# Performance work log

Hardware: AMD Instinct MI355X
Metric: run time of the kernel (lower is better)

## Reference

```python
import jax, jax.numpy as jnp
import numpy as np

BN_EPS = 1e-5

def conv1x1(x, w, b):
    # x: [B,C,H,W], w: [O,C], b: [O]
    return jnp.einsum('bchw,oc->bohw', x, w) + b[None, :, None, None]

def bn_inf(x, gamma, beta, mean, var):
    inv = gamma / jnp.sqrt(var + BN_EPS)
    return (x - mean[None, :, None, None]) * inv[None, :, None, None] + beta[None, :, None, None]

def setup_inputs() -> dict:
    key = jax.random.key(0)
    ks = jax.random.split(key, 24)
    B, Fg, Fl, Fi = 8, 256, 256, 64
    H = W = 64
    c8 = Fi // 8
    d = {}
    d['g'] = jax.random.normal(ks[0], (B, Fg, H, W), jnp.float32)
    d['x'] = jax.random.normal(ks[1], (B, Fl, H, W), jnp.float32)
    # W_g: conv1x1 + BN
    d['Wg_w'] = jax.random.normal(ks[2], (Fi, Fg), jnp.float32) * (1.0 / np.sqrt(Fg))
    d['Wg_b'] = jax.random.normal(ks[3], (Fi,), jnp.float32) * 0.02
    d['bng_gamma'] = jax.random.uniform(ks[4], (Fi,), jnp.float32, 0.5, 1.5)
    d['bng_beta'] = jax.random.normal(ks[5], (Fi,), jnp.float32) * 0.1
    d['bng_mean'] = jax.random.normal(ks[6], (Fi,), jnp.float32) * 0.1
    d['bng_var'] = jax.random.uniform(ks[7], (Fi,), jnp.float32, 0.5, 1.5)
    # W_x: conv1x1 + BN
    d['Wx_w'] = jax.random.normal(ks[8], (Fi, Fl), jnp.float32) * (1.0 / np.sqrt(Fl))
    d['Wx_b'] = jax.random.normal(ks[9], (Fi,), jnp.float32) * 0.02
    d['bnx_gamma'] = jax.random.uniform(ks[10], (Fi,), jnp.float32, 0.5, 1.5)
    d['bnx_beta'] = jax.random.normal(ks[11], (Fi,), jnp.float32) * 0.1
    d['bnx_mean'] = jax.random.normal(ks[12], (Fi,), jnp.float32) * 0.1
    d['bnx_var'] = jax.random.uniform(ks[13], (Fi,), jnp.float32, 0.5, 1.5)
    # psi: conv1x1 (Fi->1) + BN(1) + sigmoid
    d['psi_w'] = jax.random.normal(ks[14], (1, Fi), jnp.float32) * (1.0 / np.sqrt(Fi))
    d['psi_b'] = jax.random.normal(ks[15], (1,), jnp.float32) * 0.02
    d['bnp_gamma'] = jax.random.uniform(ks[16], (1,), jnp.float32, 0.5, 1.5)
    d['bnp_beta'] = jax.random.normal(ks[17], (1,), jnp.float32) * 0.1
    d['bnp_mean'] = jax.random.normal(ks[18], (1,), jnp.float32) * 0.1
    d['bnp_var'] = jax.random.uniform(ks[19], (1,), jnp.float32, 0.5, 1.5)
    # PAM convs
    d['pb_w'] = jax.random.normal(ks[20], (c8, Fi), jnp.float32) * (1.0 / np.sqrt(Fi))
    d['pb_b'] = jnp.zeros((c8,), jnp.float32)
    d['pc_w'] = jax.random.normal(ks[21], (c8, Fi), jnp.float32) * (1.0 / np.sqrt(Fi))
    d['pc_b'] = jnp.zeros((c8,), jnp.float32)
    d['pd_w'] = jax.random.normal(ks[22], (Fi, Fi), jnp.float32) * (1.0 / np.sqrt(Fi))
    d['pd_b'] = jnp.zeros((Fi,), jnp.float32)
    # scalar gates (torch inits to 0; use small nonzero to exercise the path)
    d['alpha'] = jax.random.normal(ks[23], (1,), jnp.float32) * 0.05
    d['cam_beta'] = jax.random.normal(jax.random.fold_in(key, 99), (1,), jnp.float32) * 0.05
    return d

def _cam(psi, cam_beta):
    B, C, H, W = psi.shape
    feat = psi.reshape(B, C, H * W)                       # [B,C,HW]
    att = jnp.einsum('bcn,bdn->bcd', feat, feat)          # [B,C,C]
    att_new = jnp.max(att, axis=-1, keepdims=True) - att  # max-subtract trick
    att = jax.nn.softmax(att_new, axis=-1)
    out = jnp.einsum('bcd,bdn->bcn', att, feat).reshape(B, C, H, W)
    return cam_beta[0] * out + psi

def _pam(psi, pb_w, pb_b, pc_w, pc_b, pd_w, pd_b, alpha):
    B, C, H, W = psi.shape
    HW = H * W
    fb = conv1x1(psi, pb_w, pb_b).reshape(B, -1, HW)      # [B,C/8,HW]
    fc = conv1x1(psi, pc_w, pc_b).reshape(B, -1, HW)      # [B,C/8,HW]
    energy = jnp.einsum('bki,bkj->bij', fb, fc)           # [B,HW,HW]
    att = jax.nn.softmax(energy, axis=-1)
    fd = conv1x1(psi, pd_w, pd_b).reshape(B, C, HW)       # [B,C,HW]
    out = jnp.einsum('bcj,bij->bci', fd, att).reshape(B, C, H, W)
    return alpha[0] * out + psi

def reference(g, x, Wg_w, Wg_b, bng_gamma, bng_beta, bng_mean, bng_var,
              Wx_w, Wx_b, bnx_gamma, bnx_beta, bnx_mean, bnx_var,
              psi_w, psi_b, bnp_gamma, bnp_beta, bnp_mean, bnp_var,
              pb_w, pb_b, pc_w, pc_b, pd_w, pd_b, alpha, cam_beta):
    g1 = bn_inf(conv1x1(g, Wg_w, Wg_b), bng_gamma, bng_beta, bng_mean, bng_var)
    x1 = bn_inf(conv1x1(x, Wx_w, Wx_b), bnx_gamma, bnx_beta, bnx_mean, bnx_var)
    psi = jax.nn.relu(g1 + x1)                            # [B,F_int,H,W]
    cam = _cam(psi, cam_beta)
    pam = _pam(psi, pb_w, pb_b, pc_w, pc_b, pd_w, pd_b, alpha)
    gate = bn_inf(conv1x1(cam * pam, psi_w, psi_b), bnp_gamma, bnp_beta, bnp_mean, bnp_var)
    da = jax.nn.sigmoid(gate)                             # [B,1,H,W]
    return x * da
```

## Files before the change

### kernel.cpp

```cpp
#include <hip/hip_runtime.h>
#include <hip/hip_bf16.h>
#include <math.h>

#define BB 8
#define CIN 256
#define FI 64
#define HW 4096
#define C8 8
#define EPS 1e-5f
#define LOG2E 1.4426950408889634f

typedef __attribute__((ext_vector_type(8))) short bf16x8;
typedef __attribute__((ext_vector_type(4))) float f32x4;
typedef __attribute__((ext_vector_type(4))) unsigned u32x4;
typedef unsigned short u16;

static __device__ __forceinline__ u16 f2b(float x) {
    unsigned u = __builtin_bit_cast(unsigned, x);
    return (u16)((u + 0x8000u) >> 16);
}
static __device__ __forceinline__ unsigned pk2(float a, float b) {
    unsigned ua = __builtin_bit_cast(unsigned, a);
    unsigned ub = __builtin_bit_cast(unsigned, b);
    return ((ua + 0x8000u) >> 16) | ((ub + 0x8000u) & 0xffff0000u);
}
static __device__ __forceinline__ unsigned cvtpk(float a, float b) {
    unsigned r;
    asm("v_cvt_pk_bf16_f32 %0, %1, %2" : "=v"(r) : "v"(a), "v"(b));
    return r;
}
static __device__ __forceinline__ float b2f(u16 v) {
    return __builtin_bit_cast(float, ((unsigned)v) << 16);
}

__global__ __launch_bounds__(256) void k_prep(
    const float* __restrict__ Wg, const float* __restrict__ Wgb,
    const float* __restrict__ gg, const float* __restrict__ gbeta,
    const float* __restrict__ gm, const float* __restrict__ gv,
    const float* __restrict__ Wx, const float* __restrict__ Wxb,
    const float* __restrict__ xg, const float* __restrict__ xbeta,
    const float* __restrict__ xm, const float* __restrict__ xv,
    const float* __restrict__ pbw, const float* __restrict__ pbb,
    const float* __restrict__ pcw, const float* __restrict__ pcb,
    const float* __restrict__ pdw, const float* __restrict__ pdb,
    u16* __restrict__ Wp, float* __restrict__ Cp,
    u16* __restrict__ Wcat, float* __restrict__ bcat)
{
    const int gid = blockIdx.x * 256 + threadIdx.x;
    for (int idx = gid; idx < FI * 512; idx += 4096) {
        int o = idx >> 9, k = idx & 511;
        float s, w;
        if (k < 256) { s = gg[o] * rsqrtf(gv[o] + EPS); w = Wg[o * 256 + k]; }
        else         { s = xg[o] * rsqrtf(xv[o] + EPS); w = Wx[o * 256 + k - 256]; }
        Wp[idx] = f2b(w * s);
    }
    for (int idx = gid; idx < 80 * 64; idx += 4096) {
        int row = idx >> 6, col = idx & 63;
        float w;
        if (row < 8)       w = pbw[row * 64 + col] * LOG2E;
        else if (row < 16) w = pcw[(row - 8) * 64 + col];
        else               w = pdw[(row - 16) * 64 + col];
        Wcat[idx] = f2b(w);
    }
    if (blockIdx.x == 0) {
        int tid = threadIdx.x;
        if (tid < FI) {
            float ig = gg[tid] * rsqrtf(gv[tid] + EPS);
            float ix = xg[tid] * rsqrtf(xv[tid] + EPS);
            Cp[tid] = (Wgb[tid] - gm[tid]) * ig + gbeta[tid]
                    + (Wxb[tid] - xm[tid]) * ix + xbeta[tid];
        }
        if (tid >= 64 && tid < 144) {
            int r = tid - 64;
            float bv = (r < 8) ? pbb[r] * LOG2E : (r < 16 ? pcb[r - 8] : pdb[r - 16]);
            bcat[r] = bv;
        }
    }
}

__global__ __launch_bounds__(256) void k_psi(
    const float* __restrict__ g, const float* __restrict__ x,
    const u16* __restrict__ Wp, const float* __restrict__ Cp,
    const u16* __restrict__ Wcat, const float* __restrict__ bcat,
    u16* __restrict__ psiB, u16* __restrict__ psiLo,
    u16* __restrict__ fbcT, u16* __restrict__ fdB)
{
    const int tid  = threadIdx.x;
    const int lane = tid & 63;
    const int w    = tid >> 6;
    const int n    = lane & 15;
    const int quad = lane >> 4;
    const int b    = blockIdx.y;
    const int p0   = blockIdx.x * 64;

    __shared__ u16 InT[64][72];
    __shared__ u16 Tbc[64][16];

    f32x4 acc[4];
#pragma unroll
    for (int mt = 0; mt < 4; ++mt) acc[mt] = (f32x4){0.f, 0.f, 0.f, 0.f};

    const size_t pxoff = (size_t)p0 + w * 16 + n;
#pragma unroll
    for (int kc = 0; kc < 8; ++kc) {
        const float* src = (kc < 4) ? g : x;
        const int ch0 = (kc & 3) * 64;
        const float* base = src + ((size_t)b * CIN + ch0 + quad * 8) * HW + pxoff;
#pragma unroll
        for (int ks = 0; ks < 2; ++ks) {
            const float* bp = base + (size_t)(ks * 32) * HW;
            float f0 = bp[0 * HW], f1 = bp[1 * HW], f2 = bp[2 * HW], f3 = bp[3 * HW];
            float f4 = bp[4 * HW], f5 = bp[5 * HW], f6 = bp[6 * HW], f7 = bp[7 * HW];
            u32x4 t = {pk2(f0, f1), pk2(f2, f3), pk2(f4, f5), pk2(f6, f7)};
            bf16x8 bfrag = __builtin_bit_cast(bf16x8, t);
            const int kglob = kc * 64 + ks * 32;
#pragma unroll
            for (int mt = 0; mt < 4; ++mt) {
                bf16x8 af = *(const bf16x8*)&Wp[(mt * 16 + n) * 512 + kglob + quad * 8];
                acc[mt] = __builtin_amdgcn_mfma_f32_16x16x32_bf16(
                              af, bfrag, acc[mt], 0, 0, 0);
            }
        }
    }

    float pv[4][4];
#pragma unroll
    for (int mt = 0; mt < 4; ++mt)
#pragma unroll
        for (int r = 0; r < 4; ++r) {
            int c = mt * 16 + quad * 4 + r;
            float v = acc[mt][r] + Cp[c];
            v = v > 0.f ? v : 0.f;
            pv[mt][r] = v;
            u16 hb = f2b(v);
            size_t idx = ((size_t)b * FI + c) * HW + p0 + w * 16 + n;
            psiB[idx]  = hb;
            psiLo[idx] = f2b(v - b2f(hb));
        }
#pragma unroll
    for (int mt = 0; mt < 4; ++mt) {
        *(unsigned*)&InT[w * 16 + n][mt * 16 + quad * 4]     = cvtpk(pv[mt][0], pv[mt][1]);
        *(unsigned*)&InT[w * 16 + n][mt * 16 + quad * 4 + 2] = cvtpk(pv[mt][2], pv[mt][3]);
    }
    __syncthreads();

    f32x4 facc[5];
#pragma unroll
    for (int nt = 0; nt < 5; ++nt) facc[nt] = (f32x4){0.f, 0.f, 0.f, 0.f};
#pragma unroll
    for (int ks = 0; ks < 2; ++ks) {
        bf16x8 af = *(const bf16x8*)&InT[w * 16 + n][ks * 32 + quad * 8];
#pragma unroll
        for (int nt = 0; nt < 5; ++nt) {
            bf16x8 bf = *(const bf16x8*)&Wcat[(nt * 16 + n) * FI + ks * 32 + quad * 8];
            facc[nt] = __builtin_amdgcn_mfma_f32_16x16x32_bf16(af, bf, facc[nt], 0, 0, 0);
        }
    }
    __syncthreads();

    {
        float bias = bcat[n];
#pragma unroll
        for (int r = 0; r < 4; ++r)
            Tbc[w * 16 + quad * 4 + r][n] = f2b(facc[0][r] + bias);
    }
#pragma unroll
    for (int nt = 1; nt < 5; ++nt) {
        int ch = (nt - 1) * 16 + n;
        float bias = bcat[nt * 16 + n];
        *(unsigned*)&InT[ch][w * 16 + quad * 4]     = cvtpk(facc[nt][0] + bias, facc[nt][1] + bias);
        *(unsigned*)&InT[ch][w * 16 + quad * 4 + 2] = cvtpk(facc[nt][2] + bias, facc[nt][3] + bias);
    }
    __syncthreads();
    {
        int row = tid >> 2, part = tid & 3;
        uint2 v = *(const uint2*)&Tbc[row][part * 4];
        *(uint2*)&fbcT[((size_t)b * HW + p0 + row) * 16 + part * 4] = v;
    }
#pragma unroll
    for (int rep = 0; rep < 2; ++rep) {
        int t = rep * 256 + tid;
        int ch = t >> 3, seg = t & 7;
        bf16x8 v = *(const bf16x8*)&InT[ch][seg * 8];
        *(bf16x8*)&fdB[((size_t)b * FI + ch) * HW + p0 + seg * 8] = v;
    }
}

static __device__ __forceinline__ void gram_body(
    int tid, int s, int b, int zz,
    const u16* __restrict__ psiB, const u16* __restrict__ psiLo,
    float* __restrict__ Gp)
{
    const int lane = tid & 63;
    const int w    = tid >> 6;
    const int n    = lane & 15;
    const int quad = lane >> 4;

    f32x4 acc[2];
#pragma unroll
    for (int nt = 0; nt < 2; ++nt) acc[nt] = (f32x4){0.f, 0.f, 0.f, 0.f};

    for (int ks = 0; ks < 4; ++ks) {
        const int k0 = s * 128 + ks * 32;
        const size_t ra = ((size_t)b * FI + w * 16 + n) * HW + k0 + quad * 8;
        bf16x8 ah = *(const bf16x8*)&psiB[ra];
        bf16x8 al = *(const bf16x8*)&psiLo[ra];
#pragma unroll
        for (int nt = 0; nt < 2; ++nt) {
            const size_t rb = ((size_t)b * FI + zz * 32 + nt * 16 + n) * HW + k0 + quad * 8;
            bf16x8 bh = *(const bf16x8*)&psiB[rb];
            bf16x8 bl = *(const bf16x8*)&psiLo[rb];
            acc[nt] = __builtin_amdgcn_mfma_f32_16x16x32_bf16(ah, bh, acc[nt], 0, 0, 0);
            acc[nt] = __builtin_amdgcn_mfma_f32_16x16x32_bf16(ah, bl, acc[nt], 0, 0, 0);
            acc[nt] = __builtin_amdgcn_mfma_f32_16x16x32_bf16(al, bh, acc[nt], 0, 0, 0);
        }
    }
#pragma unroll
    for (int nt = 0; nt < 2; ++nt)
#pragma unroll
        for (int r = 0; r < 4; ++r) {
            int i = w * 16 + quad * 4 + r;
            Gp[(((size_t)s * 8 + b) * 64 + i) * 64 + zz * 32 + nt * 16 + n] = acc[nt][r];
        }
}

struct PamShared {
    u16 Ks[2][68][8];
    u16 Vs[2][64][64];
    u16 Ps[4][16][64];
};

template<int P>
static __device__ __forceinline__ void pam_body(
    PamShared& sh, int tid, int b, int i0, int p,
    const u16* __restrict__ fbcT, const u16* __restrict__ fdB,
    u16* __restrict__ Opart, float* __restrict__ ml)
{
    const int lane = tid & 63;
    const int w    = tid >> 6;
    const int n    = lane & 15;
    const int quad = lane >> 4;
    constexpr int JPER = 64 / P;
    const int jstart = p * JPER, jend = jstart + JPER;

    if (tid < 16) {
        ((unsigned*)&sh.Ks[0][64][0])[tid] = 0u;
        ((unsigned*)&sh.Ks[1][64][0])[tid] = 0u;
    }

    bf16x8 qfrag = {};
    if (quad == 0)
        qfrag = *(const bf16x8*)&fbcT[((size_t)b * HW + i0 + w * 16 + n) * 16];

    const int kkey = tid >> 1, khalf = tid & 1;
    const int vch  = tid >> 3, vseg  = tid & 7;
    const int vslot = (vseg ^ (vch & 7)) << 3;
    const int pswz  = n & 7;

    const u16* kp = fbcT + ((size_t)b * HW + jstart * 64) * 16 + 8;
    const u16* vp = fdB + (size_t)b * FI * HW + jstart * 64;

    uint2 kr0 = make_uint2(0u, 0u), kr1 = make_uint2(0u, 0u);
    bf16x8 v0a, v0b, v1a, v1b;
    if (tid < 128) {
        kr0 = *(const uint2*)(kp + (size_t)kkey * 16 + khalf * 4);
        kr1 = *(const uint2*)(kp + 1024 + (size_t)kkey * 16 + khalf * 4);
    }
    v0a = *(const bf16x8*)(vp + (size_t)vch * HW + vseg * 8);
    v0b = *(const bf16x8*)(vp + (size_t)(32 + vch) * HW + vseg * 8);
    v1a = *(const bf16x8*)(vp + 64 + (size_t)vch * HW + vseg * 8);
    v1b = *(const bf16x8*)(vp + 64 + (size_t)(32 + vch) * HW + vseg * 8);

    f32x4 oacc[4];
#pragma unroll
    for (int mt = 0; mt < 4; ++mt) oacc[mt] = (f32x4){0.f, 0.f, 0.f, 0.f};
    float m = -1e30f, l = 0.f;

#define PAM_STEP(BUF)                                                           \
    {                                                                           \
        f32x4 s[4];                                                             \
        __builtin_amdgcn_s_setprio(1);                                          \
        _Pragma("unroll")                                                       \
        for (int mt = 0; mt < 4; ++mt) {                                        \
            bf16x8 af = *(const bf16x8*)&sh.Ks[BUF][mt * 16 + n + quad][0];     \
            s[mt] = __builtin_amdgcn_mfma_f32_16x16x32_bf16(                    \
                        af, qfrag, (f32x4){0.f, 0.f, 0.f, 0.f}, 0, 0, 0);       \
        }                                                                       \
        __builtin_amdgcn_s_setprio(0);                                          \
        float cm = fmaxf(fmaxf(s[0][0], s[0][1]), s[0][2]);                     \
        cm = fmaxf(fmaxf(cm, s[0][3]), s[1][0]);                                \
        cm = fmaxf(fmaxf(cm, s[1][1]), s[1][2]);                                \
        cm = fmaxf(fmaxf(cm, s[1][3]), s[2][0]);                                \
        cm = fmaxf(fmaxf(cm, s[2][1]), s[2][2]);                                \
        cm = fmaxf(fmaxf(cm, s[2][3]), s[3][0]);                                \
        cm = fmaxf(fmaxf(cm, s[3][1]), s[3][2]);                                \
        cm = fmaxf(cm, s[3][3]);                                                \
        cm = fmaxf(cm, __shfl_xor(cm, 16));                                     \
        cm = fmaxf(cm, __shfl_xor(cm, 32));                                     \
        if (__any(cm > m + 8.f)) {                                              \
            float mnew  = fmaxf(m, cm);                                         \
            float scale = __builtin_amdgcn_exp2f(m - mnew);                     \
            l *= scale;                                                         \
            _Pragma("unroll")                                                   \
            for (int mt = 0; mt < 4; ++mt) {                                    \
                oacc[mt][0] *= scale; oacc[mt][1] *= scale;                     \
                oacc[mt][2] *= scale; oacc[mt][3] *= scale;                     \
            }                                                                   \
            m = mnew;                                                           \
        }                                                                       \
        float psum = 0.f;                                                       \
        unsigned pw[4][2];                                                      \
        _Pragma("unroll")                                                       \
        for (int mt = 0; mt < 4; ++mt) {                                        \
            float e0 = __builtin_amdgcn_exp2f(s[mt][0] - m);                    \
            float e1 = __builtin_amdgcn_exp2f(s[mt][1] - m);                    \
            float e2 = __builtin_amdgcn_exp2f(s[mt][2] - m);                    \
            float e3 = __builtin_amdgcn_exp2f(s[mt][3] - m);                    \
            psum += (e0 + e1) + (e2 + e3);                                      \
            pw[mt][0] = cvtpk(e0, e1);                                          \
            pw[mt][1] = cvtpk(e2, e3);                                          \
        }                                                                       \
        l += psum;                                                              \
        _Pragma("unroll")                                                       \
        for (int mt = 0; mt < 4; ++mt) {                                        \
            int so = (((mt * 2 + (quad >> 1)) ^ pswz) << 3) + ((quad & 1) << 2);\
            *(uint2*)&sh.Ps[w][n][so] = make_uint2(pw[mt][0], pw[mt][1]);       \
        }                                                                       \
        __builtin_amdgcn_s_setprio(1);                                          \
        _Pragma("unroll")                                                       \
        for (int k0 = 0; k0 < 2; ++k0) {                                        \
            bf16x8 pf = *(const bf16x8*)&sh.Ps[w][n][((k0 * 4 + quad) ^ pswz) << 3];\
            _Pragma("unroll")                                                   \
            for (int mt = 0; mt < 4; ++mt) {                                    \
                bf16x8 vf = *(const bf16x8*)                                    \
                    &sh.Vs[BUF][mt * 16 + n][((k0 * 4 + quad) ^ pswz) << 3];    \
                oacc[mt] = __builtin_amdgcn_mfma_f32_16x16x32_bf16(             \
                               vf, pf, oacc[mt], 0, 0, 0);                      \
            }                                                                   \
        }                                                                       \
        __builtin_amdgcn_s_setprio(0);                                          \
    }

    for (int jc = jstart; jc < jend; jc += 2) {
        if (tid < 128) *(uint2*)&sh.Ks[0][kkey][khalf * 4] = kr0;
        *(bf16x8*)&sh.Vs[0][vch][vslot]      = v0a;
        *(bf16x8*)&sh.Vs[0][32 + vch][vslot] = v0b;
        if (jc + 2 < jend) {
            if (tid < 128)
                kr0 = *(const uint2*)(kp + 2048 + (size_t)kkey * 16 + khalf * 4);
            v0a = *(const bf16x8*)(vp + 128 + (size_t)vch * HW + vseg * 8);
            v0b = *(const bf16x8*)(vp + 128 + (size_t)(32 + vch) * HW + vseg * 8);
        }
        __syncthreads();
        PAM_STEP(0)

        if (tid < 128) *(uint2*)&sh.Ks[1][kkey][khalf * 4] = kr1;
        *(bf16x8*)&sh.Vs[1][vch][vslot]      = v1a;
        *(bf16x8*)&sh.Vs[1][32 + vch][vslot] = v1b;
        if (jc + 3 < jend) {
            if (tid < 128)
                kr1 = *(const uint2*)(kp + 3072 + (size_t)kkey * 16 + khalf * 4);
            v1a = *(const bf16x8*)(vp + 192 + (size_t)vch * HW + vseg * 8);
            v1b = *(const bf16x8*)(vp + 192 + (size_t)(32 + vch) * HW + vseg * 8);
        }
        kp += 2048;
        vp += 128;
        __syncthreads();
        PAM_STEP(1)
    }
#undef PAM_STEP

    l += __shfl_xor(l, 16);
    l += __shfl_xor(l, 32);
    const float rl = 1.f / l;
#pragma unroll
    for (int mt = 0; mt < 4; ++mt)
#pragma unroll
        for (int r = 0; r < 4; ++r) {
            int c = mt * 16 + quad * 4 + r;
            Opart[(((size_t)p * 8 + b) * FI + c) * HW + i0 + w * 16 + n] =
                f2b(oacc[mt][r] * rl);
        }
    if (quad == 0)
        ((float2*)ml)[((size_t)p * 8 + b) * HW + i0 + w * 16 + n] = make_float2(m, l);
}

__global__ __launch_bounds__(256) void k_pamgram(
    const u16* __restrict__ fbcT, const u16* __restrict__ fdB,
    const u16* __restrict__ psiB, const u16* __restrict__ psiLo,
    u16* __restrict__ Opart, float* __restrict__ ml, float* __restrict__ Gp)
{
    __shared__ PamShared sh;
    const int bid = blockIdx.x;
    const int tid = threadIdx.x;
    if (bid < 512) {
        gram_body(tid, bid & 31, (bid >> 5) & 7, bid >> 8, psiB, psiLo, Gp);
    } else {
        const int pid = bid - 512;
        pam_body<2>(sh, tid, pid & 7, ((pid >> 3) & 63) * 64, pid >> 9,
                    fbcT, fdB, Opart, ml);
    }
}

__global__ __launch_bounds__(256) void k_gram(
    const u16* __restrict__ psiB, const u16* __restrict__ psiLo,
    float* __restrict__ Gp)
{
    gram_body(threadIdx.x, blockIdx.x, blockIdx.y, blockIdx.z, psiB, psiLo, Gp);
}
__global__ __launch_bounds__(256) void k_pam(
    const u16* __restrict__ fbcT, const u16* __restrict__ fdB,
    u16* __restrict__ Opart, float* __restrict__ ml)
{
    __shared__ PamShared sh;
    pam_body<2>(sh, threadIdx.x, blockIdx.x, blockIdx.y * 64, blockIdx.z,
                fbcT, fdB, Opart, ml);
}

__global__ __launch_bounds__(256) void k_camsm(
    const float* __restrict__ Gp, float* __restrict__ att)
{
    const int tid = threadIdx.x, tx = tid & 63, ty = tid >> 6;
    const int b = blockIdx.x, i = blockIdx.y;
    __shared__ float part[4][64];

    float gs = 0.f;
#pragma unroll
    for (int j = 0; j < 8; ++j) {
        int s = ty * 8 + j;
        gs += Gp[(((size_t)s * 8 + b) * 64 + i) * 64 + tx];
    }
    part[ty][tx] = gs;
    __syncthreads();
    if (tid < 64) {
        float gsum = part[0][tx] + part[1][tx] + part[2][tx] + part[3][tx];
        float M = gsum;
#pragma unroll
        for (int msk = 1; msk < 64; msk <<= 1) M = fmaxf(M, __shfl_xor(M, msk));
        float a = M - gsum;
        float m2 = a;
#pragma unroll
        for (int msk = 1; msk < 64; msk <<= 1) m2 = fmaxf(m2, __shfl_xor(m2, msk));
        float p = __expf(a - m2);
        float ssum = p;
#pragma unroll
        for (int msk = 1; msk < 64; msk <<= 1) ssum += __shfl_xor(ssum, msk);
        att[((size_t)b * 64 + i) * 64 + tx] = p / ssum;
    }
}

__global__ __launch_bounds__(256) void k_final(
    const u16* __restrict__ psiB, const u16* __restrict__ psiLo,
    const float* __restrict__ att,
    const u16* __restrict__ Opart, const float* __restrict__ ml,
    const float* __restrict__ x,
    const float* __restrict__ psiw, const float* __restrict__ psib,
    const float* __restrict__ pg, const float* __restrict__ pbeta,
    const float* __restrict__ pm, const float* __restrict__ pv,
    const float* __restrict__ alpha, const float* __restrict__ camb,
    float* __restrict__ out)
{
    const int tid  = threadIdx.x;
    const int lane = tid & 63;
    const int w    = tid >> 6;
    const int n    = lane & 15;
    const int quad = lane >> 4;
    const int b = blockIdx.y, p0 = blockIdx.x * 64;

    __shared__ u16 Abf[64][64];
    __shared__ u16 tpB[64][64];
    __shared__ u16 tpLo[64][64];
    __shared__ float Wc0[64], Wc1[64], Pw[64];
    __shared__ alignas(16) float daL[64];
    __shared__ float Zp[4][64];

    {
        int c = tid >> 2, seg = tid & 3;
        const float* ap = &att[((size_t)b * 64 + c) * 64 + seg * 16];
        float4 v0 = *(const float4*)(ap);
        float4 v1 = *(const float4*)(ap + 4);
        float4 v2 = *(const float4*)(ap + 8);
        float4 v3 = *(const float4*)(ap + 12);
        float vv[16] = {v0.x, v0.y, v0.z, v0.w, v1.x, v1.y, v1.z, v1.w,
                        v2.x, v2.y, v2.z, v2.w, v3.x, v3.y, v3.z, v3.w};
#pragma unroll
        for (int j = 0; j < 8; ++j) {
            int d0 = seg * 16 + j * 2;
            int phys = (((d0 >> 3) ^ (c & 7)) << 3) | (d0 & 7);
            *(unsigned*)&Abf[c][phys] = cvtpk(vv[2 * j], vv[2 * j + 1]);
        }
    }
    {
        int px = tid & 63, grp = tid >> 6;
#pragma unroll
        for (int cc = 0; cc < 16; cc += 2) {
            int c = grp * 16 + cc;
            size_t i0 = ((size_t)b * FI + c) * HW + p0 + px;
            unsigned hb = ((unsigned)psiB[i0]) | (((unsigned)psiB[i0 + HW]) << 16);
            unsigned lb = ((unsigned)psiLo[i0]) | (((unsigned)psiLo[i0 + HW]) << 16);
            int phys = (((c >> 3) ^ (px & 7)) << 3) | (c & 7);
            *(unsigned*)&tpB[px][phys]  = hb;
            *(unsigned*)&tpLo[px][phys] = lb;
        }
    }
    if (tid < 64) {
        Pw[tid] = psiw[tid];
        float2 ml0 = ((const float2*)ml)[((size_t)0 * 8 + b) * HW + p0 + tid];
        float2 ml1 = ((const float2*)ml)[((size_t)1 * 8 + b) * HW + p0 + tid];
        float M  = fmaxf(ml0.x, ml1.x);
        float w0 = ml0.y * __builtin_amdgcn_exp2f(ml0.x - M);
        float w1 = ml1.y * __builtin_amdgcn_exp2f(ml1.x - M);
        float winv = 1.f / (w0 + w1);
        Wc0[tid] = w0 * winv; Wc1[tid] = w1 * winv;
    }
    __syncthreads();

    f32x4 acc[4];
#pragma unroll
    for (int nt = 0; nt < 4; ++nt) acc[nt] = (f32x4){0.f, 0.f, 0.f, 0.f};
#pragma unroll
    for (int ks = 0; ks < 2; ++ks) {
        int arow = w * 16 + n;
        bf16x8 af = *(const bf16x8*)&Abf[arow][((ks * 4 + quad) ^ (arow & 7)) << 3];
#pragma unroll
        for (int nt = 0; nt < 4; ++nt) {
            int brow = nt * 16 + n;
            int boff = ((ks * 4 + quad) ^ (brow & 7)) << 3;
            bf16x8 bh = *(const bf16x8*)&tpB[brow][boff];
            bf16x8 bl = *(const bf16x8*)&tpLo[brow][boff];
            acc[nt] = __builtin_amdgcn_mfma_f32_16x16x32_bf16(af, bh, acc[nt], 0, 0, 0);
            acc[nt] = __builtin_amdgcn_mfma_f32_16x16x32_bf16(af, bl, acc[nt], 0, 0, 0);
        }
    }

    const float al = alpha[0], cb = camb[0];
    float z[4] = {0.f, 0.f, 0.f, 0.f};
#pragma unroll
    for (int nt = 0; nt < 4; ++nt) {
        int px = nt * 16 + n;
        float w0 = Wc0[px], w1 = Wc1[px];
#pragma unroll
        for (int r = 0; r < 4; ++r) {
            int c = w * 16 + quad * 4 + r;
            int phys = (((c >> 3) ^ (px & 7)) << 3) | (c & 7);
            float ps  = b2f(tpB[px][phys]) + b2f(tpLo[px][phys]);
            float cam = cb * acc[nt][r] + ps;
            float oa = w0 * b2f(Opart[(((size_t)0 * 8 + b) * FI + c) * HW + p0 + px])
                     + w1 * b2f(Opart[(((size_t)1 * 8 + b) * FI + c) * HW + p0 + px]);
            float pam = al * oa + ps;
            z[nt] += Pw[c] * (cam * pam);
        }
    }
#pragma unroll
    for (int nt = 0; nt < 4; ++nt) {
        z[nt] += __shfl_xor(z[nt], 16);
        z[nt] += __shfl_xor(z[nt], 32);
    }
    if (quad == 0) {
#pragma unroll
        for (int nt = 0; nt < 4; ++nt) Zp[w][nt * 16 + n] = z[nt];
    }
    __syncthreads();
    if (tid < 64) {
        float zt = Zp[0][tid] + Zp[1][tid] + Zp[2][tid] + Zp[3][tid] + psib[0];
        float inv = pg[0] * rsqrtf(pv[0] + EPS);
        float gate = (zt - pm[0]) * inv + pbeta[0];
        daL[tid] = 1.f / (1.f + __expf(-gate));
    }
    __syncthreads();

    {
        const int pxg = tid & 15, chb = tid >> 4;
        float4 daf = *(const float4*)&daL[pxg * 4];
#pragma unroll
        for (int r = 0; r < 16; ++r) {
            int cl = chb + 16 * r;
            size_t idx = ((size_t)b * CIN + cl) * HW + p0 + pxg * 4;
            float4 xv = *(const float4*)&x[idx];
            *(float4*)&out[idx] = make_float4(xv.x * daf.x, xv.y * daf.y,
                                              xv.z * daf.z, xv.w * daf.w);
        }
    }
}

extern "C" void kernel_launch(void* const* d_in, const int* in_sizes, int n_in,
                              void* d_out, int out_size, void* d_ws, size_t ws_size,
                              hipStream_t stream)
{
    const float* g     = (const float*)d_in[0];
    const float* x     = (const float*)d_in[1];
    const float* Wg_w  = (const float*)d_in[2];
    const float* Wg_b  = (const float*)d_in[3];
    const float* bng_g = (const float*)d_in[4];
    const float* bng_b = (const float*)d_in[5];
    const float* bng_m = (const float*)d_in[6];
    const float* bng_v = (const float*)d_in[7];
    const float* Wx_w  = (const float*)d_in[8];
    const float* Wx_b  = (const float*)d_in[9];
    const float* bnx_g = (const float*)d_in[10];
    const float* bnx_b = (const float*)d_in[11];
    const float* bnx_m = (const float*)d_in[12];
    const float* bnx_v = (const float*)d_in[13];
    const float* psi_w = (const float*)d_in[14];
    const float* psi_b = (const float*)d_in[15];
    const float* bnp_g = (const float*)d_in[16];
    const float* bnp_b = (const float*)d_in[17];
    const float* bnp_m = (const float*)d_in[18];
    const float* bnp_v = (const float*)d_in[19];
    const float* pb_w  = (const float*)d_in[20];
    const float* pb_b  = (const float*)d_in[21];
    const float* pc_w  = (const float*)d_in[22];
    const float* pc_b  = (const float*)d_in[23];
    const float* pd_w  = (const float*)d_in[24];
    const float* pd_b  = (const float*)d_in[25];
    const float* alpha = (const float*)d_in[26];
    const float* camb  = (const float*)d_in[27];
    float* out = (float*)d_out;

    float* ws   = (float*)d_ws;
    u16*  psiB  = (u16*)(ws);
    u16*  psiLo = (u16*)(ws + 1048576);
    u16*  fbcT  = (u16*)(ws + 2097152);
    u16*  fdB   = (u16*)(ws + 2359296);
    float* att  = ws + 3407872;
    u16*  Wp    = (u16*)(ws + 3440640);
    float* Cp   = ws + 3457024;
    u16*  Wcat  = (u16*)(ws + 3457088);
    float* bcat = ws + 3459648;
    float* mlws = ws + 3459744;
    float* Gp   = ws + 3590816;

    const bool fused = ws_size >= (size_t)6736544 * 4;
    u16* Opart = fused ? (u16*)(ws + 4639392)
                       : (u16*)(ws + 3590816);

    k_prep<<<dim3(16), 256, 0, stream>>>(Wg_w, Wg_b, bng_g, bng_b, bng_m, bng_v,
                                         Wx_w, Wx_b, bnx_g, bnx_b, bnx_m, bnx_v,
                                         pb_w, pb_b, pc_w, pc_b, pd_w, pd_b,
                                         Wp, Cp, Wcat, bcat);
    k_psi<<<dim3(64, 8), 256, 0, stream>>>(g, x, Wp, Cp, Wcat, bcat,
                                           psiB, psiLo, fbcT, fdB);
    if (fused) {
        k_pamgram<<<dim3(1536), 256, 0, stream>>>(fbcT, fdB, psiB, psiLo,
                                                  Opart, mlws, Gp);
        k_camsm<<<dim3(8, 64), 256, 0, stream>>>(Gp, att);
    } else {
        k_gram<<<dim3(32, 8, 2), 256, 0, stream>>>(psiB, psiLo, Gp);
        k_camsm<<<dim3(8, 64), 256, 0, stream>>>(Gp, att);
        k_pam<<<dim3(8, 64, 2), 256, 0, stream>>>(fbcT, fdB, Opart, mlws);
    }
    k_final<<<dim3(64, 8), 256, 0, stream>>>(psiB, psiLo, att, Opart, mlws, x,
                                             psi_w, psi_b, bnp_g, bnp_b, bnp_m, bnp_v,
                                             alpha, camb, out);
}
```

Measured before the change: 245.6 us.

## Emit pixel-major psi copy and add vectorized 32-pixel final kernel

k_psi now also writes a transposed, pixel-major copy of psi (hi and lo bf16 parts) through shared memory, so the final kernel can load psi with coalesced 16-byte reads. A new k_final_v processes 32 pixels per block, doubling the grid, uses XOR-swizzled shared tiles, and writes the output with float4 stores. The goal is cheaper, better-coalesced loads in the final stage, paid for by extra global writes in k_psi and a larger workspace. It falls back to the old path when the workspace is too small.

```diff
diff --git a/kernel.cpp b/kernel.cpp
--- a/kernel.cpp
+++ b/kernel.cpp
@@ -83,7 +83,8 @@
     const u16* __restrict__ Wp, const float* __restrict__ Cp,
     const u16* __restrict__ Wcat, const float* __restrict__ bcat,
     u16* __restrict__ psiB, u16* __restrict__ psiLo,
-    u16* __restrict__ fbcT, u16* __restrict__ fdB)
+    u16* __restrict__ fbcT, u16* __restrict__ fdB,
+    u16* __restrict__ psiT, u16* __restrict__ psiTLo)
 {
     const int tid  = threadIdx.x;
     const int lane = tid & 63;
@@ -94,6 +95,8 @@
     const int p0   = blockIdx.x * 64;
 
     __shared__ u16 InT[64][72];
+    __shared__ u16 TpH[64][72];
+    __shared__ u16 TpL[64][72];
     __shared__ u16 Tbc[64][16];
 
     f32x4 acc[4];
@@ -124,6 +127,7 @@
     }
 
     float pv[4][4];
+    unsigned hbv[4][4], lov[4][4];
 #pragma unroll
     for (int mt = 0; mt < 4; ++mt)
 #pragma unroll
@@ -133,16 +137,34 @@
             v = v > 0.f ? v : 0.f;
             pv[mt][r] = v;
             u16 hb = f2b(v);
+            u16 lo = f2b(v - b2f(hb));
+            hbv[mt][r] = hb;
+            lov[mt][r] = lo;
             size_t idx = ((size_t)b * FI + c) * HW + p0 + w * 16 + n;
             psiB[idx]  = hb;
-            psiLo[idx] = f2b(v - b2f(hb));
+            psiLo[idx] = lo;
         }
 #pragma unroll
     for (int mt = 0; mt < 4; ++mt) {
         *(unsigned*)&InT[w * 16 + n][mt * 16 + quad * 4]     = cvtpk(pv[mt][0], pv[mt][1]);
         *(unsigned*)&InT[w * 16 + n][mt * 16 + quad * 4 + 2] = cvtpk(pv[mt][2], pv[mt][3]);
-    }
-    __syncthreads();
+        *(unsigned*)&TpH[w * 16 + n][mt * 16 + quad * 4]     = hbv[mt][0] | (hbv[mt][1] << 16);
+        *(unsigned*)&TpH[w * 16 + n][mt * 16 + quad * 4 + 2] = hbv[mt][2] | (hbv[mt][3] << 16);
+        *(unsigned*)&TpL[w * 16 + n][mt * 16 + quad * 4]     = lov[mt][0] | (lov[mt][1] << 16);
+        *(unsigned*)&TpL[w * 16 + n][mt * 16 + quad * 4 + 2] = lov[mt][2] | (lov[mt][3] << 16);
+    }
+    __syncthreads();
+
+    if (psiT != nullptr) {
+#pragma unroll
+        for (int rep = 0; rep < 2; ++rep) {
+            int t = rep * 256 + tid;
+            int row = t >> 3, seg = t & 7;
+            size_t o = ((size_t)b * HW + p0 + row) * 64 + seg * 8;
+            *(bf16x8*)&psiT[o]   = *(const bf16x8*)&TpH[row][seg * 8];
+            *(bf16x8*)&psiTLo[o] = *(const bf16x8*)&TpL[row][seg * 8];
+        }
+    }
 
     f32x4 facc[5];
 #pragma unroll
@@ -449,7 +471,143 @@
     }
 }
 
-__global__ __launch_bounds__(256) void k_final(
+__global__ __launch_bounds__(256) void k_final_v(
+    const u16* __restrict__ psiT, const u16* __restrict__ psiTLo,
+    const float* __restrict__ att,
+    const u16* __restrict__ Opart, const float* __restrict__ ml,
+    const float* __restrict__ x,
+    const float* __restrict__ psiw, const float* __restrict__ psib,
+    const float* __restrict__ pg, const float* __restrict__ pbeta,
+    const float* __restrict__ pm, const float* __restrict__ pv,
+    const float* __restrict__ alpha, const float* __restrict__ camb,
+    float* __restrict__ out)
+{
+    const int tid  = threadIdx.x;
+    const int lane = tid & 63;
+    const int w    = tid >> 6;
+    const int n    = lane & 15;
+    const int quad = lane >> 4;
+    const int b = blockIdx.y, p0 = blockIdx.x * 32;
+
+    __shared__ u16 Abf[64][64];
+    __shared__ u16 tpB[32][64];
+    __shared__ u16 tpLo[32][64];
+    __shared__ u16 OpS[2][64][40];
+    __shared__ float Wc[2][32];
+    __shared__ float Pw[64];
+    __shared__ alignas(16) float daL[32];
+    __shared__ float Zp[4][32];
+
+    {
+        int c = tid >> 2, seg = tid & 3;
+        const float* ap = &att[((size_t)b * 64 + c) * 64 + seg * 16];
+        float4 v0 = *(const float4*)(ap);
+        float4 v1 = *(const float4*)(ap + 4);
+        float4 v2 = *(const float4*)(ap + 8);
+        float4 v3 = *(const float4*)(ap + 12);
+        float vv[16] = {v0.x, v0.y, v0.z, v0.w, v1.x, v1.y, v1.z, v1.w,
+                        v2.x, v2.y, v2.z, v2.w, v3.x, v3.y, v3.z, v3.w};
+#pragma unroll
+        for (int j = 0; j < 8; ++j) {
+            int d0 = seg * 16 + j * 2;
+            int phys = (((d0 >> 3) ^ (c & 7)) << 3) | (d0 & 7);
+            *(unsigned*)&Abf[c][phys] = cvtpk(vv[2 * j], vv[2 * j + 1]);
+        }
+    }
+    {
+        int row = tid >> 3, seg = tid & 7;
+        size_t o = ((size_t)b * HW + p0 + row) * 64 + seg * 8;
+        int phys = ((seg ^ (row & 7)) << 3);
+        *(bf16x8*)&tpB[row][phys]  = *(const bf16x8*)&psiT[o];
+        *(bf16x8*)&tpLo[row][phys] = *(const bf16x8*)&psiTLo[o];
+    }
+#pragma unroll
+    for (int rep = 0; rep < 2; ++rep) {
+        int cid = rep * 256 + tid;
+        int pp = cid >> 8, c = (cid >> 2) & 63, sg = cid & 3;
+        *(bf16x8*)&OpS[pp][c][sg * 8] =
+            *(const bf16x8*)&Opart[(((size_t)pp * 8 + b) * FI + c) * HW + p0 + sg * 8];
+    }
+    if (tid < 64) Pw[tid] = psiw[tid];
+    if (tid < 32) {
+        float2 ml0 = ((const float2*)ml)[((size_t)0 * 8 + b) * HW + p0 + tid];
+        float2 ml1 = ((const float2*)ml)[((size_t)1 * 8 + b) * HW + p0 + tid];
+        float M  = fmaxf(ml0.x, ml1.x);
+        float w0 = ml0.y * __builtin_amdgcn_exp2f(ml0.x - M);
+        float w1 = ml1.y * __builtin_amdgcn_exp2f(ml1.x - M);
+        float winv = 1.f / (w0 + w1);
+        Wc[0][tid] = w0 * winv; Wc[1][tid] = w1 * winv;
+    }
+    __syncthreads();
+
+    f32x4 acc[2];
+#pragma unroll
+    for (int nt = 0; nt < 2; ++nt) acc[nt] = (f32x4){0.f, 0.f, 0.f, 0.f};
+#pragma unroll
+    for (int ks = 0; ks < 2; ++ks) {
+        int arow = w * 16 + n;
+        bf16x8 af = *(const bf16x8*)&Abf[arow][((ks * 4 + quad) ^ (arow & 7)) << 3];
+#pragma unroll
+        for (int nt = 0; nt < 2; ++nt) {
+            int brow = nt * 16 + n;
+            int boff = ((ks * 4 + quad) ^ (brow & 7)) << 3;
+            bf16x8 bh = *(const bf16x8*)&tpB[brow][boff];
+            bf16x8 bl = *(const bf16x8*)&tpLo[brow][boff];
+            acc[nt] = __builtin_amdgcn_mfma_f32_16x16x32_bf16(af, bh, acc[nt], 0, 0, 0);
+            acc[nt] = __builtin_amdgcn_mfma_f32_16x16x32_bf16(af, bl, acc[nt], 0, 0, 0);
+        }
+    }
+
+    const float al = alpha[0], cb = camb[0];
+    float z[2] = {0.f, 0.f};
+#pragma unroll
+    for (int nt = 0; nt < 2; ++nt) {
+        int px = nt * 16 + n;
+        float w0 = Wc[0][px], w1 = Wc[1][px];
+#pragma unroll
+        for (int r = 0; r < 4; ++r) {
+            int c = w * 16 + quad * 4 + r;
+            int phys = (((c >> 3) ^ (px & 7)) << 3) | (c & 7);
+            float ps  = b2f(tpB[px][phys]) + b2f(tpLo[px][phys]);
+            float cam = cb * acc[nt][r] + ps;
+            float oa = w0 * b2f(OpS[0][c][px]) + w1 * b2f(OpS[1][c][px]);
+            float pam = al * oa + ps;
+            z[nt] += Pw[c] * (cam * pam);
+        }
+    }
+#pragma unroll
+    for (int nt = 0; nt < 2; ++nt) {
+        z[nt] += __shfl_xor(z[nt], 16);
+        z[nt] += __shfl_xor(z[nt], 32);
+    }
+    if (quad == 0) {
+#pragma unroll
+        for (int nt = 0; nt < 2; ++nt) Zp[w][nt * 16 + n] = z[nt];
+    }
+    __syncthreads();
+    if (tid < 32) {
+        float zt = Zp[0][tid] + Zp[1][tid] + Zp[2][tid] + Zp[3][tid] + psib[0];
+        float inv = pg[0] * rsqrtf(pv[0] + EPS);
+        float gate = (zt - pm[0]) * inv + pbeta[0];
+        daL[tid] = 1.f / (1.f + __expf(-gate));
+    }
+    __syncthreads();
+
+    {
+        const int pxg = tid & 7, chb = tid >> 3;
+        float4 daf = *(const float4*)&daL[pxg * 4];
+#pragma unroll
+        for (int r = 0; r < 8; ++r) {
+            int cl = chb + 32 * r;
+            size_t idx = ((size_t)b * CIN + cl) * HW + p0 + pxg * 4;
+            float4 xv = *(const float4*)&x[idx];
+            *(float4*)&out[idx] = make_float4(xv.x * daf.x, xv.y * daf.y,
+                                              xv.z * daf.z, xv.w * daf.w);
+        }
+    }
+}
+
+__global__ __launch_bounds__(256) void k_final_s(
     const u16* __restrict__ psiB, const u16* __restrict__ psiLo,
     const float* __restrict__ att,
     const u16* __restrict__ Opart, const float* __restrict__ ml,
@@ -618,29 +776,34 @@
     float* out = (float*)d_out;
 
     float* ws   = (float*)d_ws;
-    u16*  psiB  = (u16*)(ws);
-    u16*  psiLo = (u16*)(ws + 1048576);
-    u16*  fbcT  = (u16*)(ws + 2097152);
-    u16*  fdB   = (u16*)(ws + 2359296);
-    float* att  = ws + 3407872;
-    u16*  Wp    = (u16*)(ws + 3440640);
-    float* Cp   = ws + 3457024;
-    u16*  Wcat  = (u16*)(ws + 3457088);
-    float* bcat = ws + 3459648;
-    float* mlws = ws + 3459744;
-    float* Gp   = ws + 3590816;
-
-    const bool fused = ws_size >= (size_t)6736544 * 4;
-    u16* Opart = fused ? (u16*)(ws + 4639392)
-                       : (u16*)(ws + 3590816);
+    u16*  psiB   = (u16*)(ws);
+    u16*  psiLo  = (u16*)(ws + 1048576);
+    u16*  fbcT   = (u16*)(ws + 2097152);
+    u16*  fdB    = (u16*)(ws + 2359296);
+    float* att   = ws + 3407872;
+    u16*  Wp     = (u16*)(ws + 3440640);
+    float* Cp    = ws + 3457024;
+    u16*  Wcat   = (u16*)(ws + 3457088);
+    float* bcat  = ws + 3459648;
+    float* mlws  = ws + 3459744;
+    float* Gp    = ws + 3590816;
+    u16*  psiT   = (u16*)(ws + 6736544);
+    u16*  psiTL  = (u16*)(ws + 7785120);
+
+    const bool wsB = ws_size >= (size_t)6736544 * 4;
+    const bool wsA = ws_size >= (size_t)8833696 * 4;
+    u16* Opart = wsB ? (u16*)(ws + 4639392)
+                     : (u16*)(ws + 3590816);
 
     k_prep<<<dim3(16), 256, 0, stream>>>(Wg_w, Wg_b, bng_g, bng_b, bng_m, bng_v,
                                          Wx_w, Wx_b, bnx_g, bnx_b, bnx_m, bnx_v,
                                          pb_w, pb_b, pc_w, pc_b, pd_w, pd_b,
                                          Wp, Cp, Wcat, bcat);
     k_psi<<<dim3(64, 8), 256, 0, stream>>>(g, x, Wp, Cp, Wcat, bcat,
-                                           psiB, psiLo, fbcT, fdB);
-    if (fused) {
+                                           psiB, psiLo, fbcT, fdB,
+                                           wsA ? psiT : nullptr,
+                                           wsA ? psiTL : nullptr);
+    if (wsB) {
         k_pamgram<<<dim3(1536), 256, 0, stream>>>(fbcT, fdB, psiB, psiLo,
                                                   Opart, mlws, Gp);
         k_camsm<<<dim3(8, 64), 256, 0, stream>>>(Gp, att);
@@ -649,7 +812,13 @@
         k_camsm<<<dim3(8, 64), 256, 0, stream>>>(Gp, att);
         k_pam<<<dim3(8, 64, 2), 256, 0, stream>>>(fbcT, fdB, Opart, mlws);
     }
-    k_final<<<dim3(64, 8), 256, 0, stream>>>(psiB, psiLo, att, Opart, mlws, x,
-                                             psi_w, psi_b, bnp_g, bnp_b, bnp_m, bnp_v,
-                                             alpha, camb, out);
-}
+    if (wsA) {
+        k_final_v<<<dim3(128, 8), 256, 0, stream>>>(psiT, psiTL, att, Opart, mlws, x,
+                                                    psi_w, psi_b, bnp_g, bnp_b,
+                                                    bnp_m, bnp_v, alpha, camb, out);
+    } else {
+        k_final_s<<<dim3(64, 8), 256, 0, stream>>>(psiB, psiLo, att, Opart, mlws, x,
+                                                   psi_w, psi_b, bnp_g, bnp_b,
+                                                   bnp_m, bnp_v, alpha, camb, out);
+    }
+}
```

Result: no change. 245.0 us (-0.2%).
